# Kernel tuning notes

Measured on AMD Instinct MI355X. Metric: run time of the kernel, lower is better.

Reference implementation:

```python
import jax, jax.numpy as jnp
import numpy as np

N_NODES = 50000
N_EDGES = 1_600_000
IN_DIM = 6
EMB = 64
EDGE_DIM = 1
L = 4
BN_EPS = 1e-5


def _bn_relu(x, gamma, beta):
    # BatchNorm1d in training mode: biased batch stats over the row dim.
    mu = jnp.mean(x, axis=0)
    var = jnp.var(x, axis=0)
    xhat = (x - mu) * jax.lax.rsqrt(var + BN_EPS)
    return jax.nn.relu(xhat * gamma + beta)


def setup_inputs() -> dict:
    key = jax.random.key(0)
    ks = jax.random.split(key, 32)
    s = 0.1
    inp = {
        "x": jax.random.normal(ks[0], (N_NODES, IN_DIM), jnp.float32),
        "edge_index": jax.random.randint(ks[1], (2, N_EDGES), 0, N_NODES),
        "edge_attr": jax.random.normal(ks[2], (N_EDGES, EDGE_DIM), jnp.float32),
        "lin_in_W": jax.random.normal(ks[3], (IN_DIM, EMB)) * s,
        "lin_in_b": jnp.zeros((EMB,)),
        # per-layer stacked params, leading dim L
        "msg_W1": jax.random.normal(ks[4], (L, 2 * EMB + EDGE_DIM, EMB)) * s,
        "msg_b1": jnp.zeros((L, EMB)),
        "msg_g1": jnp.ones((L, EMB)),
        "msg_be1": jnp.zeros((L, EMB)),
        "msg_W2": jax.random.normal(ks[5], (L, EMB, EMB)) * s,
        "msg_b2": jnp.zeros((L, EMB)),
        "msg_g2": jnp.ones((L, EMB)),
        "msg_be2": jnp.zeros((L, EMB)),
        "upd_W1": jax.random.normal(ks[6], (L, 2 * EMB, EMB)) * s,
        "upd_b1": jnp.zeros((L, EMB)),
        "upd_g1": jnp.ones((L, EMB)),
        "upd_be1": jnp.zeros((L, EMB)),
        "upd_W2": jax.random.normal(ks[7], (L, EMB, EMB)) * s,
        "upd_b2": jnp.zeros((L, EMB)),
        "upd_g2": jnp.ones((L, EMB)),
        "upd_be2": jnp.zeros((L, EMB)),
        "pred_W": jax.random.normal(ks[8], (EMB, 1)) * s,
        "pred_b": jnp.zeros((1,)),
    }
    return inp


def reference(x, edge_index, edge_attr, lin_in_W, lin_in_b,
              msg_W1, msg_b1, msg_g1, msg_be1, msg_W2, msg_b2, msg_g2, msg_be2,
              upd_W1, upd_b1, upd_g1, upd_be1, upd_W2, upd_b2, upd_g2, upd_be2,
              pred_W, pred_b):
    n = x.shape[0]
    src = edge_index[0]  # j (source)
    dst = edge_index[1]  # i (target / aggregation index)

    h = x @ lin_in_W + lin_in_b  # (n, d)
    for l in range(L):
        h_i = h[dst]                              # (e, d) destination feats
        h_j = h[src]                              # (e, d) source feats
        m = jnp.concatenate([h_i, h_j, edge_attr], axis=-1)  # (e, 2d+de)
        m = _bn_relu(m @ msg_W1[l] + msg_b1[l], msg_g1[l], msg_be1[l])
        m = _bn_relu(m @ msg_W2[l] + msg_b2[l], msg_g2[l], msg_be2[l])
        aggr = jax.ops.segment_sum(m, dst, num_segments=n)   # (n, d)
        u = jnp.concatenate([h, aggr], axis=-1)              # (n, 2d)
        u = _bn_relu(u @ upd_W1[l] + upd_b1[l], upd_g1[l], upd_be1[l])
        u = _bn_relu(u @ upd_W2[l] + upd_b2[l], upd_g2[l], upd_be2[l])
        h = h + u  # residual
    out = h @ pred_W + pred_b
    return out.reshape(-1)
```

## Files before the change

### kernel.cpp

```cpp
#include <hip/hip_runtime.h>
#include <hip/hip_bf16.h>


#define BN_EPS 1e-5f
#define NSH 128
#define TPB 4
#define LYS 72
#define LW1S 168
#define LW2S 68
#define ASW 66

typedef __attribute__((ext_vector_type(4))) short short4v;
typedef __attribute__((ext_vector_type(8))) short short8;
typedef __attribute__((ext_vector_type(16))) float floatx16;

#define MFMA32 __builtin_amdgcn_mfma_f32_32x32x16_bf16

__device__ __forceinline__ short f2bs(float f) {
  union { float f; unsigned u; } x; x.f = f;
  unsigned r = x.u + 0x7fffu + ((x.u >> 16) & 1u);
  return (short)(r >> 16);
}
__device__ __forceinline__ short f2bs_fast(float f) {
  union { float f; unsigned u; } x; x.f = f;
  return (short)((x.u + 0x8000u) >> 16);
}
__device__ __forceinline__ float bs2f(short s) {
  union { unsigned u; float f; } x;
  x.u = ((unsigned)(unsigned short)s) << 16;
  return x.f;
}


__global__ void lin_in_kernel(const float* __restrict__ x,
                              const float* __restrict__ W,
                              const float* __restrict__ b, float* __restrict__ h,
                              short* __restrict__ hb, int N) {
  int gid = blockIdx.x * blockDim.x + threadIdx.x;
  if (gid >= N * 64) return;
  int n = gid >> 6, o = gid & 63;
  float acc = b[o];
#pragma unroll
  for (int k = 0; k < 6; ++k) acc += x[n * 6 + k] * W[k * 64 + o];
  h[gid] = acc;
  hb[gid] = f2bs(acc);
}

__global__ void deg_kernel(const int* __restrict__ ei, int* __restrict__ deg,
                           int E) {
  int gid = blockIdx.x * blockDim.x + threadIdx.x;
  if (gid < E) atomicAdd(&deg[ei[E + gid]], 1);
}

__global__ void scan_kernel(const int* __restrict__ deg, int* __restrict__ offs,
                            int N) {
  __shared__ int s[1024];
  int t = threadIdx.x;
  int chunk = (N + 1023) >> 10;
  int lo = t * chunk, hi = lo + chunk;
  if (hi > N) hi = N;
  if (lo > N) lo = N;
  int tot = 0;
  for (int i = lo; i < hi; ++i) tot += deg[i];
  s[t] = tot;
  __syncthreads();
  for (int off = 1; off < 1024; off <<= 1) {
    int v = (t >= off) ? s[t - off] : 0;
    __syncthreads();
    s[t] += v;
    __syncthreads();
  }
  int run = s[t] - tot;
  for (int i = lo; i < hi; ++i) {
    offs[i] = run;
    run += deg[i];
  }
}

__global__ void fill_kernel(const int* __restrict__ ei,
                            const int* __restrict__ offs, int* __restrict__ cnt,
                            int* __restrict__ sorted, int E) {
  int gid = blockIdx.x * blockDim.x + threadIdx.x;
  if (gid >= E) return;
  int d = ei[E + gid];
  int pos = offs[d] + atomicAdd(&cnt[d], 1);
  sorted[pos] = gid;
}

__global__ void gather_edges_kernel(const int* __restrict__ ei,
                                    const int* __restrict__ sorted,
                                    const float* __restrict__ ea,
                                    int* __restrict__ dd, int* __restrict__ ds,
                                    short* __restrict__ es, int E, int Epad) {
  int i = blockIdx.x * 256 + threadIdx.x;
  if (i >= Epad) return;
  if (i < E) {
    int e = sorted[i];
    dd[i] = ei[E + e];
    ds[i] = ei[e];
    es[i] = f2bs(ea[e]);
  } else {
    dd[i] = -1;
    ds[i] = 0;
    es[i] = 0;
  }
}

__global__ void pack_w1_kernel(const float* __restrict__ W,
                               short* __restrict__ Wt, int L_) {
  int i = blockIdx.x * 256 + threadIdx.x;
  if (i >= L_ * 64 * 160) return;
  int k = i % 160, n = (i / 160) % 64, l = i / (160 * 64);
  Wt[i] = (k < 129) ? f2bs(W[((size_t)l * 129 + k) * 64 + n]) : (short)0;
}

__global__ void pack_w2_kernel(const float* __restrict__ W,
                               short* __restrict__ Wt, int L_) {
  int i = blockIdx.x * 256 + threadIdx.x;
  if (i >= L_ * 64 * 64) return;
  int k = i % 64, n = (i / 64) % 64, l = i / 4096;
  Wt[i] = f2bs(W[((size_t)l * 64 + k) * 64 + n]);
}

__global__ void bn_finalize_kernel(const float* __restrict__ shards,
                                   const float* __restrict__ gamma,
                                   const float* __restrict__ beta, float cnt,
                                   float* __restrict__ ac) {
  int o = threadIdx.x;
  float s = 0.f, q = 0.f;
  for (int i = 0; i < NSH; ++i) {
    s += shards[i * 128 + o];
    q += shards[i * 128 + 64 + o];
  }
  float mu = s / cnt;
  float var = fmaxf(q / cnt - mu * mu, 0.f);
  float r = rsqrtf(var + BN_EPS);
  float g = gamma[o];
  ac[o] = g * r;
  ac[64 + o] = beta[o] - mu * g * r;
}

__global__ void bn_finalize_pack1(const float* __restrict__ shards,
                                  const float* __restrict__ gamma,
                                  const float* __restrict__ beta, float cnt,
                                  const float* __restrict__ W,
                                  const float* __restrict__ b,
                                  short* __restrict__ Wt,
                                  float* __restrict__ bs) {
  __shared__ float sa[64];
  int t = threadIdx.x;
  if (t < 64) {
    float s = 0.f, q = 0.f;
    for (int i = 0; i < NSH; ++i) {
      s += shards[i * 128 + t];
      q += shards[i * 128 + 64 + t];
    }
    float mu = s / cnt;
    float var = fmaxf(q / cnt - mu * mu, 0.f);
    float r = rsqrtf(var + BN_EPS);
    float a = gamma[t] * r;
    float c = beta[t] - mu * a;
    sa[t] = a;
    if (blockIdx.x == 0) bs[t] = a * b[t] + c;
  }
  __syncthreads();
  int i = blockIdx.x * 256 + t;
  if (i < 64 * 160) {
    int k = i % 160, n = i / 160;
    Wt[i] = (k < 129) ? f2bs(W[k * 64 + n] * sa[n]) : (short)0;
  }
}

__global__ void bn_finalize_pack2(const float* __restrict__ shards,
                                  const float* __restrict__ gamma,
                                  const float* __restrict__ beta, float cnt,
                                  const float* __restrict__ W,
                                  const float* __restrict__ b,
                                  short* __restrict__ Wt,
                                  float* __restrict__ bs) {
  __shared__ float sa[64];
  int t = threadIdx.x;
  if (t < 64) {
    float s = 0.f, q = 0.f;
    for (int i = 0; i < NSH; ++i) {
      s += shards[i * 128 + t];
      q += shards[i * 128 + 64 + t];
    }
    float mu = s / cnt;
    float var = fmaxf(q / cnt - mu * mu, 0.f);
    float r = rsqrtf(var + BN_EPS);
    float a = gamma[t] * r;
    float c = beta[t] - mu * a;
    sa[t] = a;
    if (blockIdx.x == 0) bs[t] = a * b[t] + c;
  }
  __syncthreads();
  int i = blockIdx.x * 256 + t;
  if (i < 64 * 64) {
    int k = i % 64, n = i / 64;
    Wt[i] = f2bs(W[k * 64 + n] * sa[n]);
  }
}


__device__ __forceinline__ void stage_w1(const short* __restrict__ Wt,
                                         short* Lw, int t) {
#pragma unroll
  for (int i = 0; i < 5; ++i) {
    int c = t + i * 256;
    int col = c / 20, ch = c % 20;
    *(short8*)&Lw[col * LW1S + ch * 8] = *(const short8*)&Wt[col * 160 + ch * 8];
  }
}
__device__ __forceinline__ void stage_w2(const short* __restrict__ Wt,
                                         short* Lw, int t) {
#pragma unroll
  for (int i = 0; i < 2; ++i) {
    int c = t + i * 256;
    int col = c >> 3, ch = c & 7;
    *(short8*)&Lw[col * LW2S + ch * 8] = *(const short8*)&Wt[col * 64 + ch * 8];
  }
}

__device__ __forceinline__ void gemm1_32(const short* __restrict__ hbf,
                                         const short* Lw1,
                                         const float* __restrict__ bias, int d,
                                         int sx, short eav, int me, int hl,
                                         floatx16 acc[2]) {
  const short* hd = hbf + (size_t)d * 64 + hl * 8;
  const short* hs = hbf + (size_t)sx * 64 + hl * 8;
  short8 A[8];
#pragma unroll
  for (int kc = 0; kc < 4; ++kc) A[kc] = *(const short8*)(hd + kc * 16);
#pragma unroll
  for (int kc = 0; kc < 4; ++kc) A[4 + kc] = *(const short8*)(hs + kc * 16);
  short8 a8 = {0, 0, 0, 0, 0, 0, 0, 0};
  if (hl == 0) a8[0] = eav;
#pragma unroll
  for (int nt = 0; nt < 2; ++nt) {
    int col = nt * 32 + me;
    float bv = bias[col];
    floatx16 a;
#pragma unroll
    for (int r = 0; r < 16; ++r) a[r] = bv;
    const short* wp = Lw1 + col * LW1S + hl * 8;
#pragma unroll
    for (int kc = 0; kc < 8; ++kc) {
      short8 B = *(const short8*)(wp + kc * 16);
      a = MFMA32(A[kc], B, a, 0, 0, 0);
    }
    short8 B8 = *(const short8*)(wp + 128);
    a = MFMA32(a8, B8, a, 0, 0, 0);
    acc[nt] = a;
  }
}

__device__ __forceinline__ void gemm1T_32(const short* __restrict__ hbf,
                                          const short* Lw1, int d, int sx,
                                          short eav, int me, int hl,
                                          floatx16 acc[2]) {
  const short* hd = hbf + (size_t)d * 64 + hl * 8;
  const short* hs = hbf + (size_t)sx * 64 + hl * 8;
  short8 Bf[8];
#pragma unroll
  for (int kc = 0; kc < 4; ++kc) Bf[kc] = *(const short8*)(hd + kc * 16);
#pragma unroll
  for (int kc = 0; kc < 4; ++kc) Bf[4 + kc] = *(const short8*)(hs + kc * 16);
  short8 b8 = {0, 0, 0, 0, 0, 0, 0, 0};
  if (hl == 0) b8[0] = eav;
#pragma unroll
  for (int nt = 0; nt < 2; ++nt) {
    floatx16 a;
#pragma unroll
    for (int r = 0; r < 16; ++r) a[r] = 0.f;
    const short* wp = Lw1 + (nt * 32 + me) * LW1S + hl * 8;
#pragma unroll
    for (int kc = 0; kc < 8; ++kc) {
      short8 A = *(const short8*)(wp + kc * 16);
      a = MFMA32(A, Bf[kc], a, 0, 0, 0);
    }
    short8 A8 = *(const short8*)(wp + 128);
    a = MFMA32(A8, b8, a, 0, 0, 0);
    acc[nt] = a;
  }
}

__device__ __forceinline__ void write_z(short* Lz, const floatx16 acc[2],
                                        const float b1v[2][16], int w, int me,
                                        int hl) {
#pragma unroll
  for (int nt = 0; nt < 2; ++nt)
#pragma unroll
    for (int g4 = 0; g4 < 4; ++g4) {
      int n1b = nt * 32 + 8 * g4 + 4 * hl;
      short4v pk;
#pragma unroll
      for (int j = 0; j < 4; ++j) {
        int r = g4 * 4 + j;
        pk[j] = f2bs_fast(fmaxf(acc[nt][r] + b1v[nt][r], 0.f));
      }
      *(short4v*)&Lz[(w * 32 + me) * LYS + n1b] = pk;
    }
}

__device__ __forceinline__ void gemm2_32(const short* Lz, const short* Lw2,
                                         const float* __restrict__ bias, int w,
                                         int me, int hl, floatx16 acc[2]) {
  short8 Z[4];
  const short* zp = &Lz[(w * 32 + me) * LYS + hl * 8];
#pragma unroll
  for (int kc = 0; kc < 4; ++kc) Z[kc] = *(const short8*)(zp + kc * 16);
#pragma unroll
  for (int nt = 0; nt < 2; ++nt) {
    int col = nt * 32 + me;
    float bv = bias[col];
    floatx16 a;
#pragma unroll
    for (int r = 0; r < 16; ++r) a[r] = bv;
    const short* wp = Lw2 + col * LW2S + hl * 8;
#pragma unroll
    for (int kc = 0; kc < 4; ++kc) {
      short8 B = *(const short8*)(wp + kc * 16);
      a = MFMA32(Z[kc], B, a, 0, 0, 0);
    }
    acc[nt] = a;
  }
}

__device__ __forceinline__ void stats32_acc(const floatx16 acc[2], int idx0,
                                            int w, int hl, int E, bool full,
                                            float sa[2], float qa[2]) {
#pragma unroll
  for (int nt = 0; nt < 2; ++nt) {
    float s = 0.f, q = 0.f;
#pragma unroll
    for (int r = 0; r < 16; ++r) {
      float v = acc[nt][r];
      if (!full) {
        int row = (r & 3) + 8 * (r >> 2) + 4 * hl;
        if (idx0 + w * 32 + row >= E) v = 0.f;
      }
      s += v;
      q += v * v;
    }
    s += __shfl_down(s, 32, 64);
    q += __shfl_down(q, 32, 64);
    sa[nt] += s;
    qa[nt] += q;
  }
}

__device__ __forceinline__ void stats_epilogue(float sred[4][128],
                                               const float sa[2],
                                               const float qa[2], int w,
                                               int lane, int t,
                                               float* __restrict__ stat,
                                               int shard) {
  if (lane < 32) {
#pragma unroll
    for (int nt = 0; nt < 2; ++nt) {
      sred[w][nt * 32 + lane] = sa[nt];
      sred[w][64 + nt * 32 + lane] = qa[nt];
    }
  }
  __syncthreads();
  if (t < 128) {
    float v = sred[0][t] + sred[1][t] + sred[2][t] + sred[3][t];
    atomicAdd(&stat[(size_t)shard * 128 + t], v);
  }
}


__global__ __launch_bounds__(256) void edge_pass_a(
    const short* __restrict__ hbf, const short* __restrict__ Wt1,
    const float* __restrict__ b1, const int* __restrict__ dd,
    const int* __restrict__ dsr, const short* __restrict__ es,
    float* __restrict__ stat, int E, int Epad) {
  __shared__ __align__(16) short Lw1[64 * LW1S];
  __shared__ float sred[4][128];
  int t = threadIdx.x;
  stage_w1(Wt1, Lw1, t);
  __syncthreads();
  int w = t >> 6, lane = t & 63, me = lane & 31, hl = lane >> 5;
  float sa[2] = {0.f, 0.f}, qa[2] = {0.f, 0.f};
  for (int it = 0; it < TPB; ++it) {
    int idx0 = (blockIdx.x * TPB + it) * 128;
    if (idx0 >= Epad) break;
    int eg = idx0 + w * 32 + me;
    int d = dd[eg];
    int dc = d < 0 ? 0 : d;
    int sx = dsr[eg];
    short eav = es[eg];
    floatx16 acc[2];
    gemm1_32(hbf, Lw1, b1, dc, sx, eav, me, hl, acc);
    stats32_acc(acc, idx0, w, hl, E, idx0 + 128 <= E, sa, qa);
  }
  stats_epilogue(sred, sa, qa, w, lane, t, stat, blockIdx.x & (NSH - 1));
}

__global__ __launch_bounds__(256) void edge_pass_b(
    const short* __restrict__ hbf, const short* __restrict__ Wt1s,
    const float* __restrict__ b1s, const int* __restrict__ dd,
    const int* __restrict__ dsr, const short* __restrict__ es,
    const short* __restrict__ Wt2, const float* __restrict__ b2,
    float* __restrict__ stat, int E, int Epad) {
  __shared__ __align__(16) short Lw1[64 * LW1S];
  __shared__ __align__(16) short Lw2[64 * LW2S];
  __shared__ __align__(16) short Lz[128 * LYS];
  __shared__ float sred[4][128];
  int t = threadIdx.x;
  stage_w1(Wt1s, Lw1, t);
  stage_w2(Wt2, Lw2, t);
  __syncthreads();
  int w = t >> 6, lane = t & 63, me = lane & 31, hl = lane >> 5;
  float b1v[2][16];
#pragma unroll
  for (int nt = 0; nt < 2; ++nt)
#pragma unroll
    for (int r = 0; r < 16; ++r)
      b1v[nt][r] = b1s[nt * 32 + (r & 3) + 8 * (r >> 2) + 4 * hl];
  float sa[2] = {0.f, 0.f}, qa[2] = {0.f, 0.f};
  for (int it = 0; it < TPB; ++it) {
    int idx0 = (blockIdx.x * TPB + it) * 128;
    if (idx0 >= Epad) break;
    int eg = idx0 + w * 32 + me;
    int d = dd[eg];
    int dc = d < 0 ? 0 : d;
    int sx = dsr[eg];
    short eav = es[eg];
    floatx16 acc[2];
    gemm1T_32(hbf, Lw1, dc, sx, eav, me, hl, acc);
    write_z(Lz, acc, b1v, w, me, hl);
    floatx16 acc2[2];
    gemm2_32(Lz, Lw2, b2, w, me, hl, acc2);
    stats32_acc(acc2, idx0, w, hl, E, idx0 + 128 <= E, sa, qa);
  }
  stats_epilogue(sred, sa, qa, w, lane, t, stat, blockIdx.x & (NSH - 1));
}

__global__ __launch_bounds__(256) void edge_pass_c(
    const short* __restrict__ hbf, const short* __restrict__ Wt1s,
    const float* __restrict__ b1s, const int* __restrict__ dd,
    const int* __restrict__ dsr, const short* __restrict__ es,
    const short* __restrict__ Wt2s, const float* __restrict__ b2s,
    float* __restrict__ aggr, int E, int Epad) {
  __shared__ __align__(16) short Lw1[64 * LW1S];
  __shared__ __align__(16) short Lw2[64 * LW2S];
  __shared__ __align__(16) short Lz[128 * LYS];
  __shared__ int sdst[128];
  int t = threadIdx.x;
  stage_w1(Wt1s, Lw1, t);
  stage_w2(Wt2s, Lw2, t);
  __syncthreads();
  int w = t >> 6, lane = t & 63, me = lane & 31, hl = lane >> 5;
  float b1v[2][16];
#pragma unroll
  for (int nt = 0; nt < 2; ++nt)
#pragma unroll
    for (int r = 0; r < 16; ++r)
      b1v[nt][r] = b1s[nt * 32 + (r & 3) + 8 * (r >> 2) + 4 * hl];
  for (int it = 0; it < TPB; ++it) {
    int idx0 = (blockIdx.x * TPB + it) * 128;
    if (idx0 >= Epad) break;
    if (t < 128) sdst[t] = dd[idx0 + t];
    int eg = idx0 + w * 32 + me;
    int d = dd[eg];
    int dc = d < 0 ? 0 : d;
    int sx = dsr[eg];
    short eav = es[eg];
    floatx16 acc[2];
    gemm1T_32(hbf, Lw1, dc, sx, eav, me, hl, acc);
    write_z(Lz, acc, b1v, w, me, hl);
    floatx16 acc2[2];
    gemm2_32(Lz, Lw2, b2s, w, me, hl, acc2);
    __syncthreads();
    int sb = w * 32;
    float s0 = 0.f, s1 = 0.f;
    int d2 = sdst[sb + 4 * hl];
#pragma unroll
    for (int g4 = 0; g4 < 4; ++g4) {
#pragma unroll
      for (int j = 0; j < 4; ++j) {
        int r = g4 * 4 + j;
        s0 += fmaxf(acc2[0][r], 0.f);
        s1 += fmaxf(acc2[1][r], 0.f);
        int offn;
        if (j == 3)
          offn = (g4 == 3) ? -1 : 8 * (g4 + 1) + 4 * hl;
        else
          offn = 8 * g4 + 4 * hl + j + 1;
        int dn = (offn < 0) ? -2 : sdst[sb + offn];
        if (d2 != dn) {
          if (d2 >= 0) {
            atomicAdd(&aggr[(size_t)d2 * 64 + me], s0);
            atomicAdd(&aggr[(size_t)d2 * 64 + me + 32], s1);
          }
          s0 = 0.f;
          s1 = 0.f;
        }
        d2 = dn;
      }
    }
    __syncthreads();
  }
}


__device__ __forceinline__ void gemm_r2c8(const float* __restrict__ As,
                                          const float* __restrict__ W, int K,
                                          int rg, int cg, float acc[2][8]) {
  const float* ap = As + rg * 2;
  const float* wp = W + cg * 8;
#pragma unroll 4
  for (int k = 0; k < K; ++k) {
    float2 a = *(const float2*)&ap[k * ASW];
    float4 w0 = *(const float4*)&wp[k * 64];
    float4 w1 = *(const float4*)&wp[k * 64 + 4];
    float wv[8] = {w0.x, w0.y, w0.z, w0.w, w1.x, w1.y, w1.z, w1.w};
#pragma unroll
    for (int j = 0; j < 8; ++j) {
      acc[0][j] += a.x * wv[j];
      acc[1][j] += a.y * wv[j];
    }
  }
}

__device__ __forceinline__ void stats_r2c8(const float acc[2][8],
                                           float* __restrict__ shard, int t,
                                           int cg) {
  float s[8], q[8];
#pragma unroll
  for (int j = 0; j < 8; ++j) {
    s[j] = acc[0][j] + acc[1][j];
    q[j] = acc[0][j] * acc[0][j] + acc[1][j] * acc[1][j];
  }
#pragma unroll
  for (int off = 32; off >= 8; off >>= 1) {
#pragma unroll
    for (int j = 0; j < 8; ++j) {
      s[j] += __shfl_down(s[j], off, 64);
      q[j] += __shfl_down(q[j], off, 64);
    }
  }
  if (((t & 63) >> 3) == 0) {
#pragma unroll
    for (int j = 0; j < 8; ++j) {
      atomicAdd(&shard[cg * 8 + j], s[j]);
      atomicAdd(&shard[64 + cg * 8 + j], q[j]);
    }
  }
}

__global__ __launch_bounds__(256) void node_gemm1_v3(
    const float* __restrict__ h, const float* __restrict__ aggr,
    const float* __restrict__ W, const float* __restrict__ b,
    float* __restrict__ u1, float* __restrict__ stat, int N) {
  __shared__ __align__(16) float As[128 * ASW];
  int n0 = blockIdx.x * 64;
  int t = threadIdx.x;
  int c = t & 63, g = t >> 6;
  for (int n = g; n < 64; n += 4) {
    int idx = n0 + n;
    bool v = idx < N;
    As[c * ASW + n] = v ? h[(size_t)idx * 64 + c] : 0.f;
    As[(64 + c) * ASW + n] = v ? aggr[(size_t)idx * 64 + c] : 0.f;
  }
  __syncthreads();
  int rg = t >> 3, cg = t & 7;
  float acc[2][8];
#pragma unroll
  for (int i = 0; i < 2; ++i)
#pragma unroll
    for (int j = 0; j < 8; ++j) acc[i][j] = b[cg * 8 + j];
  gemm_r2c8(As, W, 128, rg, cg, acc);
#pragma unroll
  for (int i = 0; i < 2; ++i) {
    int idx = n0 + rg * 2 + i;
    if (idx < N) {
      *(float4*)&u1[(size_t)idx * 64 + cg * 8] =
          make_float4(acc[i][0], acc[i][1], acc[i][2], acc[i][3]);
      *(float4*)&u1[(size_t)idx * 64 + cg * 8 + 4] =
          make_float4(acc[i][4], acc[i][5], acc[i][6], acc[i][7]);
    } else {
#pragma unroll
      for (int j = 0; j < 8; ++j) acc[i][j] = 0.f;
    }
  }
  stats_r2c8(acc, stat + (size_t)(blockIdx.x & (NSH - 1)) * 128, t, cg);
}

__global__ __launch_bounds__(256) void node_gemm2_v3(
    const float* __restrict__ u1, const float* __restrict__ ac,
    const float* __restrict__ W, const float* __restrict__ b,
    float* __restrict__ u2, float* __restrict__ stat, int N) {
  __shared__ __align__(16) float As[64 * ASW];
  int n0 = blockIdx.x * 64;
  int t = threadIdx.x;
  int c = t & 63, g = t >> 6;
  float a1 = ac[c], c1 = ac[64 + c];
  for (int n = g; n < 64; n += 4) {
    int idx = n0 + n;
    bool v = idx < N;
    As[c * ASW + n] = v ? fmaxf(u1[(size_t)idx * 64 + c] * a1 + c1, 0.f) : 0.f;
  }
  __syncthreads();
  int rg = t >> 3, cg = t & 7;
  float acc[2][8];
#pragma unroll
  for (int i = 0; i < 2; ++i)
#pragma unroll
    for (int j = 0; j < 8; ++j) acc[i][j] = b[cg * 8 + j];
  gemm_r2c8(As, W, 64, rg, cg, acc);
#pragma unroll
  for (int i = 0; i < 2; ++i) {
    int idx = n0 + rg * 2 + i;
    if (idx < N) {
      *(float4*)&u2[(size_t)idx * 64 + cg * 8] =
          make_float4(acc[i][0], acc[i][1], acc[i][2], acc[i][3]);
      *(float4*)&u2[(size_t)idx * 64 + cg * 8 + 4] =
          make_float4(acc[i][4], acc[i][5], acc[i][6], acc[i][7]);
    } else {
#pragma unroll
      for (int j = 0; j < 8; ++j) acc[i][j] = 0.f;
    }
  }
  stats_r2c8(acc, stat + (size_t)(blockIdx.x & (NSH - 1)) * 128, t, cg);
}

__global__ void residual_kernel(float* __restrict__ h, short* __restrict__ hb,
                                const float* __restrict__ u2,
                                const float* __restrict__ ac, int total) {
  int gid = blockIdx.x * blockDim.x + threadIdx.x;
  if (gid >= total) return;
  int o = gid & 63;
  float v = u2[gid] * ac[o] + ac[64 + o];
  float nv = h[gid] + fmaxf(v, 0.f);
  h[gid] = nv;
  hb[gid] = f2bs(nv);
}

__global__ void pred_kernel(const float* __restrict__ h,
                            const float* __restrict__ W,
                            const float* __restrict__ b,
                            float* __restrict__ out, int N) {
  int n = blockIdx.x * blockDim.x + threadIdx.x;
  if (n >= N) return;
  float acc = b[0];
  const float* hr = h + (size_t)n * 64;
#pragma unroll
  for (int o = 0; o < 64; ++o) acc += hr[o] * W[o];
  out[n] = acc;
}


extern "C" void kernel_launch(void* const* d_in, const int* in_sizes, int n_in,
                              void* d_out, int out_size, void* d_ws,
                              size_t ws_size, hipStream_t stream) {
  const float* x = (const float*)d_in[0];
  const int* ei = (const int*)d_in[1];
  const float* ea = (const float*)d_in[2];
  const float* lin_W = (const float*)d_in[3];
  const float* lin_b = (const float*)d_in[4];
  const float* msg_W1 = (const float*)d_in[5];
  const float* msg_b1 = (const float*)d_in[6];
  const float* msg_g1 = (const float*)d_in[7];
  const float* msg_be1 = (const float*)d_in[8];
  const float* msg_W2 = (const float*)d_in[9];
  const float* msg_b2 = (const float*)d_in[10];
  const float* msg_g2 = (const float*)d_in[11];
  const float* msg_be2 = (const float*)d_in[12];
  const float* upd_W1 = (const float*)d_in[13];
  const float* upd_b1 = (const float*)d_in[14];
  const float* upd_g1 = (const float*)d_in[15];
  const float* upd_be1 = (const float*)d_in[16];
  const float* upd_W2 = (const float*)d_in[17];
  const float* upd_b2 = (const float*)d_in[18];
  const float* upd_g2 = (const float*)d_in[19];
  const float* upd_be2 = (const float*)d_in[20];
  const float* pred_W = (const float*)d_in[21];
  const float* pred_b = (const float*)d_in[22];
  float* out = (float*)d_out;

  const int N = in_sizes[0] / 6;
  const int E = in_sizes[1] / 2;
  const int L = 4;
  const int Epad = ((E + 127) / 128) * 128;

  char* p = (char*)d_ws;
  auto alloc = [&](size_t bytes) {
    void* r = (void*)p;
    p += (bytes + 255) & ~(size_t)255;
    return r;
  };
  float* h = (float*)alloc((size_t)N * 64 * 4);
  short* hb = (short*)alloc((size_t)N * 64 * 2);
  float* aggr = (float*)alloc((size_t)N * 64 * 4);
  float* stats = (float*)alloc((size_t)4 * NSH * 128 * 4);
  float* acu1 = (float*)alloc(128 * 4);
  float* acu2 = (float*)alloc(128 * 4);
  float* b1s = (float*)alloc(64 * 4);
  float* b2s = (float*)alloc(64 * 4);
  float* u1 = (float*)alloc((size_t)N * 64 * 4);
  float* u2 = (float*)alloc((size_t)N * 64 * 4);
  int* deg = (int*)alloc((size_t)N * 4);
  int* offs = (int*)alloc((size_t)N * 4);
  int* cnt = (int*)alloc((size_t)N * 4);
  int* sorted = (int*)alloc((size_t)E * 4);
  int* dd = (int*)alloc((size_t)Epad * 4);
  int* dsr = (int*)alloc((size_t)Epad * 4);
  short* es = (short*)alloc((size_t)Epad * 2);
  short* Wt1 = (short*)alloc((size_t)L * 64 * 160 * 2);
  short* Wt2 = (short*)alloc((size_t)L * 64 * 64 * 2);
  short* Wt1s = (short*)alloc((size_t)64 * 160 * 2);
  short* Wt2s = (short*)alloc((size_t)64 * 64 * 2);

  const int B = 256;
  const size_t REG = (size_t)NSH * 128;
  int gridE256 = (E + 255) / 256;
  int NT = Epad / 128;
  int gridEdge = (NT + TPB - 1) / TPB;
  int gridM64 = (N + 63) / 64;
  int gridN64 = (N * 64 + B - 1) / B;
  int gridN = (N + B - 1) / B;

  hipMemsetAsync(deg, 0, (size_t)N * 4, stream);
  hipMemsetAsync(cnt, 0, (size_t)N * 4, stream);
  lin_in_kernel<<<gridN64, B, 0, stream>>>(x, lin_W, lin_b, h, hb, N);
  deg_kernel<<<gridE256, B, 0, stream>>>(ei, deg, E);
  scan_kernel<<<1, 1024, 0, stream>>>(deg, offs, N);
  fill_kernel<<<gridE256, B, 0, stream>>>(ei, offs, cnt, sorted, E);
  gather_edges_kernel<<<(Epad + 255) / 256, B, 0, stream>>>(ei, sorted, ea, dd,
                                                            dsr, es, E, Epad);
  pack_w1_kernel<<<(L * 64 * 160 + 255) / 256, B, 0, stream>>>(msg_W1, Wt1, L);
  pack_w2_kernel<<<(L * 64 * 64 + 255) / 256, B, 0, stream>>>(msg_W2, Wt2, L);

  for (int l = 0; l < L; ++l) {
    const short* Wt1l = Wt1 + (size_t)l * 64 * 160;
    const short* Wt2l = Wt2 + (size_t)l * 64 * 64;
    const float* U1 = upd_W1 + (size_t)l * 128 * 64;
    const float* U2 = upd_W2 + (size_t)l * 64 * 64;
    hipMemsetAsync(aggr, 0, (size_t)N * 64 * 4 + (size_t)4 * REG * 4, stream);
    edge_pass_a<<<gridEdge, 256, 0, stream>>>(hb, Wt1l, msg_b1 + l * 64, dd,
                                              dsr, es, stats, E, Epad);
    bn_finalize_pack1<<<(64 * 160 + 255) / 256, B, 0, stream>>>(
        stats, msg_g1 + l * 64, msg_be1 + l * 64, (float)E,
        msg_W1 + (size_t)l * 129 * 64, msg_b1 + l * 64, Wt1s, b1s);
    edge_pass_b<<<gridEdge, 256, 0, stream>>>(hb, Wt1s, b1s, dd, dsr, es, Wt2l,
                                              msg_b2 + l * 64, stats + REG, E,
                                              Epad);
    bn_finalize_pack2<<<(64 * 64 + 255) / 256, B, 0, stream>>>(
        stats + REG, msg_g2 + l * 64, msg_be2 + l * 64, (float)E,
        msg_W2 + (size_t)l * 64 * 64, msg_b2 + l * 64, Wt2s, b2s);
    edge_pass_c<<<gridEdge, 256, 0, stream>>>(hb, Wt1s, b1s, dd, dsr, es, Wt2s,
                                              b2s, aggr, E, Epad);
    node_gemm1_v3<<<gridM64, 256, 0, stream>>>(h, aggr, U1, upd_b1 + l * 64,
                                               u1, stats + 2 * REG, N);
    bn_finalize_kernel<<<1, 64, 0, stream>>>(stats + 2 * REG, upd_g1 + l * 64,
                                             upd_be1 + l * 64, (float)N, acu1);
    node_gemm2_v3<<<gridM64, 256, 0, stream>>>(u1, acu1, U2, upd_b2 + l * 64,
                                               u2, stats + 3 * REG, N);
    bn_finalize_kernel<<<1, 64, 0, stream>>>(stats + 3 * REG, upd_g2 + l * 64,
                                             upd_be2 + l * 64, (float)N, acu2);
    residual_kernel<<<gridN64, B, 0, stream>>>(h, hb, u2, acu2, N * 64);
  }
  pred_kernel<<<gridN, B, 0, stream>>>(h, pred_W, pred_b, out, N);
}
```

Baseline: 1.948 ms.

## Software-pipeline edge gathers and drop block barriers in edge aggregation pass

Restructures the edge_pass_c loop so that the gathered node-feature fragments for the next 128-edge tile, and the edge indices two tiles ahead, are loaded into registers while the current tile's MFMAs run. Destination indices move into a per-wave shared array, which removes the two block-wide __syncthreads per iteration. The aim is to hide global gather latency behind compute and cut synchronisation stalls. In exchange, register pressure rises from the double-buffered fragments, which may lower occupancy.

```diff
diff --git a/kernel.cpp b/kernel.cpp
--- a/kernel.cpp
+++ b/kernel.cpp
@@ -255,34 +255,46 @@
   }
 }
 
+__device__ __forceinline__ void load_frag(const short* __restrict__ hbf, int d,
+                                          int sx, int hl, short8 Bf[8]) {
+  int dc = d < 0 ? 0 : d;
+  const short* hd = hbf + (size_t)dc * 64 + hl * 8;
+  const short* hs = hbf + (size_t)sx * 64 + hl * 8;
+#pragma unroll
+  for (int kc = 0; kc < 4; ++kc) Bf[kc] = *(const short8*)(hd + kc * 16);
+#pragma unroll
+  for (int kc = 0; kc < 4; ++kc) Bf[4 + kc] = *(const short8*)(hs + kc * 16);
+}
+
+__device__ __forceinline__ void gemm1T_mfma(const short* Lw1,
+                                            const short8 Bf[8], short eav,
+                                            int me, int hl, floatx16 acc[2]) {
+  short8 b8 = {0, 0, 0, 0, 0, 0, 0, 0};
+  if (hl == 0) b8[0] = eav;
+#pragma unroll
+  for (int nt = 0; nt < 2; ++nt) {
+    floatx16 a;
+#pragma unroll
+    for (int r = 0; r < 16; ++r) a[r] = 0.f;
+    const short* wp = Lw1 + (nt * 32 + me) * LW1S + hl * 8;
+#pragma unroll
+    for (int kc = 0; kc < 8; ++kc) {
+      short8 A = *(const short8*)(wp + kc * 16);
+      a = MFMA32(A, Bf[kc], a, 0, 0, 0);
+    }
+    short8 A8 = *(const short8*)(wp + 128);
+    a = MFMA32(A8, b8, a, 0, 0, 0);
+    acc[nt] = a;
+  }
+}
+
 __device__ __forceinline__ void gemm1T_32(const short* __restrict__ hbf,
                                           const short* Lw1, int d, int sx,
                                           short eav, int me, int hl,
                                           floatx16 acc[2]) {
-  const short* hd = hbf + (size_t)d * 64 + hl * 8;
-  const short* hs = hbf + (size_t)sx * 64 + hl * 8;
   short8 Bf[8];
-#pragma unroll
-  for (int kc = 0; kc < 4; ++kc) Bf[kc] = *(const short8*)(hd + kc * 16);
-#pragma unroll
-  for (int kc = 0; kc < 4; ++kc) Bf[4 + kc] = *(const short8*)(hs + kc * 16);
-  short8 b8 = {0, 0, 0, 0, 0, 0, 0, 0};
-  if (hl == 0) b8[0] = eav;
-#pragma unroll
-  for (int nt = 0; nt < 2; ++nt) {
-    floatx16 a;
-#pragma unroll
-    for (int r = 0; r < 16; ++r) a[r] = 0.f;
-    const short* wp = Lw1 + (nt * 32 + me) * LW1S + hl * 8;
-#pragma unroll
-    for (int kc = 0; kc < 8; ++kc) {
-      short8 A = *(const short8*)(wp + kc * 16);
-      a = MFMA32(A, Bf[kc], a, 0, 0, 0);
-    }
-    short8 A8 = *(const short8*)(wp + 128);
-    a = MFMA32(A8, b8, a, 0, 0, 0);
-    acc[nt] = a;
-  }
+  load_frag(hbf, d, sx, hl, Bf);
+  gemm1T_mfma(Lw1, Bf, eav, me, hl, acc);
 }
 
 __device__ __forceinline__ void write_z(short* Lz, const floatx16 acc[2],
@@ -447,61 +459,94 @@
   __shared__ __align__(16) short Lw1[64 * LW1S];
   __shared__ __align__(16) short Lw2[64 * LW2S];
   __shared__ __align__(16) short Lz[128 * LYS];
-  __shared__ int sdst[128];
+  __shared__ int sdstw[4][32];
   int t = threadIdx.x;
   stage_w1(Wt1s, Lw1, t);
   stage_w2(Wt2s, Lw2, t);
+  int w = t >> 6, lane = t & 63, me = lane & 31, hl = lane >> 5;
+  const int base0 = blockIdx.x * TPB * 128;
+  int d_c, sx_c, d_n, sx_n;
+  short eav_c, eav_n;
+  {
+    int eg = base0 + w * 32 + me;
+    d_c = dd[eg];
+    sx_c = dsr[eg];
+    eav_c = es[eg];
+    int i1 = base0 + 128;
+    if (i1 < Epad) {
+      d_n = dd[i1 + w * 32 + me];
+      sx_n = dsr[i1 + w * 32 + me];
+      eav_n = es[i1 + w * 32 + me];
+    } else {
+      d_n = -1;
+      sx_n = 0;
+      eav_n = 0;
+    }
+  }
+  short8 Bf_c[8], Bf_n[8];
+  load_frag(hbf, d_c, sx_c, hl, Bf_c);
   __syncthreads();
-  int w = t >> 6, lane = t & 63, me = lane & 31, hl = lane >> 5;
   float b1v[2][16];
 #pragma unroll
   for (int nt = 0; nt < 2; ++nt)
 #pragma unroll
     for (int r = 0; r < 16; ++r)
       b1v[nt][r] = b1s[nt * 32 + (r & 3) + 8 * (r >> 2) + 4 * hl];
+#pragma unroll
   for (int it = 0; it < TPB; ++it) {
-    int idx0 = (blockIdx.x * TPB + it) * 128;
-    if (idx0 >= Epad) break;
-    if (t < 128) sdst[t] = dd[idx0 + t];
-    int eg = idx0 + w * 32 + me;
-    int d = dd[eg];
-    int dc = d < 0 ? 0 : d;
-    int sx = dsr[eg];
-    short eav = es[eg];
-    floatx16 acc[2];
-    gemm1T_32(hbf, Lw1, dc, sx, eav, me, hl, acc);
-    write_z(Lz, acc, b1v, w, me, hl);
-    floatx16 acc2[2];
-    gemm2_32(Lz, Lw2, b2s, w, me, hl, acc2);
-    __syncthreads();
-    int sb = w * 32;
-    float s0 = 0.f, s1 = 0.f;
-    int d2 = sdst[sb + 4 * hl];
-#pragma unroll
-    for (int g4 = 0; g4 < 4; ++g4) {
-#pragma unroll
-      for (int j = 0; j < 4; ++j) {
-        int r = g4 * 4 + j;
-        s0 += fmaxf(acc2[0][r], 0.f);
-        s1 += fmaxf(acc2[1][r], 0.f);
-        int offn;
-        if (j == 3)
-          offn = (g4 == 3) ? -1 : 8 * (g4 + 1) + 4 * hl;
-        else
-          offn = 8 * g4 + 4 * hl + j + 1;
-        int dn = (offn < 0) ? -2 : sdst[sb + offn];
-        if (d2 != dn) {
-          if (d2 >= 0) {
-            atomicAdd(&aggr[(size_t)d2 * 64 + me], s0);
-            atomicAdd(&aggr[(size_t)d2 * 64 + me + 32], s1);
+    int idx0 = base0 + it * 128;
+    if (idx0 < Epad) {
+      bool nv = (idx0 + 128) < Epad;
+      if (nv) load_frag(hbf, d_n, sx_n, hl, Bf_n);
+      int d_2 = -1, sx_2 = 0;
+      short eav_2 = 0;
+      int i2 = idx0 + 256;
+      if (it + 2 < TPB && i2 < Epad) {
+        d_2 = dd[i2 + w * 32 + me];
+        sx_2 = dsr[i2 + w * 32 + me];
+        eav_2 = es[i2 + w * 32 + me];
+      }
+      if (lane < 32) sdstw[w][lane] = d_c;
+      floatx16 acc[2];
+      gemm1T_mfma(Lw1, Bf_c, eav_c, me, hl, acc);
+      write_z(Lz, acc, b1v, w, me, hl);
+      floatx16 acc2[2];
+      gemm2_32(Lz, Lw2, b2s, w, me, hl, acc2);
+      float s0 = 0.f, s1 = 0.f;
+      int d2 = sdstw[w][4 * hl];
+#pragma unroll
+      for (int g4 = 0; g4 < 4; ++g4) {
+#pragma unroll
+        for (int j = 0; j < 4; ++j) {
+          int r = g4 * 4 + j;
+          s0 += fmaxf(acc2[0][r], 0.f);
+          s1 += fmaxf(acc2[1][r], 0.f);
+          int offn;
+          if (j == 3)
+            offn = (g4 == 3) ? -1 : 8 * (g4 + 1) + 4 * hl;
+          else
+            offn = 8 * g4 + 4 * hl + j + 1;
+          int dn = (offn < 0) ? -2 : sdstw[w][offn];
+          if (d2 != dn) {
+            if (d2 >= 0) {
+              atomicAdd(&aggr[(size_t)d2 * 64 + me], s0);
+              atomicAdd(&aggr[(size_t)d2 * 64 + me + 32], s1);
+            }
+            s0 = 0.f;
+            s1 = 0.f;
           }
-          s0 = 0.f;
-          s1 = 0.f;
+          d2 = dn;
         }
-        d2 = dn;
       }
-    }
-    __syncthreads();
+#pragma unroll
+      for (int kc = 0; kc < 8; ++kc) Bf_c[kc] = Bf_n[kc];
+      d_c = d_n;
+      sx_c = sx_n;
+      eav_c = eav_n;
+      d_n = d_2;
+      sx_n = sx_2;
+      eav_n = eav_2;
+    }
   }
 }
 
```

Result: faster. 1.870 ms (median of 2 runs) (-4.0%).
